# Optimization experiments

Measured on AMD Instinct MI355X. Metric: run time of the kernel, lower is better.

## Reference

```python
import jax, jax.numpy as jnp
import numpy as np

DIM, HEADS, WS, SS = 256, 8, 4, 2
B, D, H, W = 2, 16, 56, 56


def _rel_pos_index(ws):
    coords = np.stack(np.meshgrid(np.arange(ws), np.arange(ws), np.arange(ws), indexing='ij'))
    flat = coords.reshape(3, -1)                      # [3, n]
    rel = (flat[:, :, None] - flat[:, None, :]).transpose(1, 2, 0).astype(np.int64)  # [n,n,3]
    rel[..., 0] += ws - 1; rel[..., 1] += ws - 1; rel[..., 2] += ws - 1
    rel[..., 0] *= (2 * ws - 1) ** 2
    rel[..., 1] *= (2 * ws - 1)
    return rel.sum(-1)                                # [n, n]


def _attn_mask(d, h, w, ws, ss):
    # dims are divisible by ws here, so padded dims == dims (matches torch ceil-pad)
    img = np.zeros((d, h, w))
    sl = (slice(0, -ws), slice(-ws, -ss), slice(-ss, None))
    cnt = 0
    for dsl in sl:
        for hsl in sl:
            for wsl in sl:
                img[dsl, hsl, wsl] = cnt
                cnt += 1
    mw = img.reshape(d // ws, ws, h // ws, ws, w // ws, ws)
    mw = mw.transpose(0, 2, 4, 1, 3, 5).reshape(-1, ws ** 3)   # [nW, n]
    diff = mw[:, None, :] - mw[:, :, None]
    return np.where(diff != 0, -100.0, 0.0).astype(np.float32)  # [nW, n, n]


def _window_partition(x, ws):
    b, d, h, w, c = x.shape
    x = x.reshape(b, d // ws, ws, h // ws, ws, w // ws, ws, c)
    return x.transpose(0, 1, 3, 5, 2, 4, 6, 7).reshape(-1, ws ** 3, c)


def _window_reverse(win, ws, b, d, h, w, c):
    x = win.reshape(b, d // ws, h // ws, w // ws, ws, ws, ws, c)
    return x.transpose(0, 1, 4, 2, 5, 3, 6, 7).reshape(b, d, h, w, c)


def _ln(x, g, b, eps=1e-5):
    mu = x.mean(-1, keepdims=True)
    var = ((x - mu) ** 2).mean(-1, keepdims=True)
    return (x - mu) * jax.lax.rsqrt(var + eps) * g + b


def setup_inputs() -> dict:
    key = jax.random.key(0)
    ks = jax.random.split(key, 8)
    s = 0.02
    return {
        'x': jax.random.normal(ks[0], (B, D, H, W, DIM), jnp.float32),
        'norm1_g': jnp.ones((DIM,), jnp.float32),
        'norm1_b': jnp.zeros((DIM,), jnp.float32),
        'qkv_w': jax.random.normal(ks[1], (DIM, 3 * DIM), jnp.float32) * s,
        'qkv_b': jnp.zeros((3 * DIM,), jnp.float32),
        'proj_w': jax.random.normal(ks[2], (DIM, DIM), jnp.float32) * s,
        'proj_b': jnp.zeros((DIM,), jnp.float32),
        'rpb_table': jax.random.normal(ks[3], ((2 * WS - 1) ** 3, HEADS), jnp.float32) * s,
        'norm2_g': jnp.ones((DIM,), jnp.float32),
        'norm2_b': jnp.zeros((DIM,), jnp.float32),
        'fc1_w': jax.random.normal(ks[4], (DIM, 4 * DIM), jnp.float32) * s,
        'fc1_b': jnp.zeros((4 * DIM,), jnp.float32),
        'fc2_w': jax.random.normal(ks[5], (4 * DIM, DIM), jnp.float32) * s,
        'fc2_b': jnp.zeros((DIM,), jnp.float32),
    }


def reference(x, norm1_g, norm1_b, qkv_w, qkv_b, proj_w, proj_b, rpb_table,
              norm2_g, norm2_b, fc1_w, fc1_b, fc2_w, fc2_b):
    b, d, h, w, c = x.shape
    nh, ws, ss = HEADS, WS, SS
    hd = c // nh
    shortcut = x

    xn = _ln(x, norm1_g, norm1_b)
    xs = jnp.roll(xn, shift=(-ss, -ss, -ss), axis=(1, 2, 3))
    xw = _window_partition(xs, ws)            # [B_, n, c]
    B_, n, _ = xw.shape

    qkv = (xw @ qkv_w + qkv_b).reshape(B_, n, 3, nh, hd).transpose(2, 0, 3, 1, 4)
    q, k, v = qkv[0], qkv[1], qkv[2]          # [B_, nh, n, hd]
    attn = jnp.einsum('bhqd,bhkd->bhqk', q * (hd ** -0.5), k)

    rpi = jnp.asarray(_rel_pos_index(ws).reshape(-1))
    bias = rpb_table[rpi].reshape(n, n, nh).transpose(2, 0, 1)  # [nh, n, n]
    attn = attn + bias[None]

    mask = jnp.asarray(_attn_mask(d, h, w, ws, ss))             # [nW, n, n]
    nW = mask.shape[0]
    attn = attn.reshape(B_ // nW, nW, nh, n, n) + mask[None, :, None]
    attn = jax.nn.softmax(attn.reshape(B_, nh, n, n), axis=-1)

    out = jnp.einsum('bhqk,bhkd->bhqd', attn, v).transpose(0, 2, 1, 3).reshape(B_, n, c)
    out = out @ proj_w + proj_b

    xr = _window_reverse(out, ws, b, d, h, w, c)
    xr = jnp.roll(xr, shift=(ss, ss, ss), axis=(1, 2, 3))
    x1 = shortcut + xr

    y = _ln(x1, norm2_g, norm2_b)
    y = jax.nn.gelu(y @ fc1_w + fc1_b, approximate=False) @ fc2_w + fc2_b
    return x1 + y
```

## Files before the change

kernel.cpp:

```cpp
#include <hip/hip_runtime.h>
#include <math.h>


using f32x4  = __attribute__((ext_vector_type(4))) float;
using bf16x8 = __attribute__((ext_vector_type(8))) short;

#define MFMA16 __builtin_amdgcn_mfma_f32_16x16x32_bf16

__device__ __forceinline__ short f2bf(float f) {
  unsigned u = __builtin_bit_cast(unsigned, f);
  u += 0x7fffu + ((u >> 16) & 1u);
  return (short)(u >> 16);
}

__device__ __forceinline__ float gelu_f(float v) {
  const float u = 1.5957691216057308f * v * (1.f + 0.044715f * v * v);
  const float e = __expf(u);
  return v - v * __builtin_amdgcn_rcpf(e + 1.f);
}

#define GLDS16(g, l) __builtin_amdgcn_global_load_lds(                        \
    (__attribute__((address_space(1))) void*)(g),                             \
    (__attribute__((address_space(3))) void*)(l), 16, 0, 0)

__global__ void transpose_all_k(const float* __restrict__ qkv_w,
                                const float* __restrict__ proj_w,
                                const float* __restrict__ fc1_w,
                                const float* __restrict__ fc2_w,
                                short* __restrict__ o_qkv,
                                short* __restrict__ o_proj,
                                short* __restrict__ o_fc1,
                                short* __restrict__ o_fc2) {
  int bid = blockIdx.x;
  const float* in; short* out; int K, N;
  if (bid < 768)       { in = qkv_w;  out = o_qkv;  K = 256;  N = 768; }
  else if (bid < 1024) { in = proj_w; out = o_proj; K = 256;  N = 256;  bid -= 768; }
  else if (bid < 2048) { in = fc1_w;  out = o_fc1;  K = 256;  N = 1024; bid -= 1024; }
  else                 { in = fc2_w;  out = o_fc2;  K = 1024; N = 256;  bid -= 2048; }
  const int idx = bid * 256 + threadIdx.x;
  const int k = idx / N, n = idx % N;
  out[(size_t)n * K + k] = f2bf(in[idx]);
}

__global__ __launch_bounds__(256) void ln1_part_k(
    const float* __restrict__ x, const float* __restrict__ g,
    const float* __restrict__ bta, short* __restrict__ xw) {
  const int wave = threadIdx.x >> 6, lane = threadIdx.x & 63;
  const int row = blockIdx.x * 4 + wave;
  const int win = row >> 6, tok = row & 63;
  const int b = win / 784, wi = win % 784;
  const int wd = wi / 196, wh = (wi / 14) % 14, ww = wi % 14;
  const int tz = tok >> 4, ty = (tok >> 2) & 3, tx = tok & 3;
  const int gd = (wd * 4 + tz + 2) & 15;
  int gh = wh * 4 + ty + 2; if (gh >= 56) gh -= 56;
  int gw = ww * 4 + tx + 2; if (gw >= 56) gw -= 56;
  const size_t src = ((((size_t)b * 16 + gd) * 56 + gh) * 56 + gw) * 256;
  const float4 v = ((const float4*)(x + src))[lane];
  float s = v.x + v.y + v.z + v.w;
#pragma unroll
  for (int m = 1; m < 64; m <<= 1) s += __shfl_xor(s, m);
  const float mean = s * (1.f / 256.f);
  const float dx = v.x - mean, dy = v.y - mean, dz = v.z - mean, dw = v.w - mean;
  float q = dx * dx + dy * dy + dz * dz + dw * dw;
#pragma unroll
  for (int m = 1; m < 64; m <<= 1) q += __shfl_xor(q, m);
  const float rstd = rsqrtf(q * (1.f / 256.f) + 1e-5f);
  const float4 gg = ((const float4*)g)[lane];
  const float4 bb = ((const float4*)bta)[lane];
  short4 o;
  o.x = f2bf(dx * rstd * gg.x + bb.x);
  o.y = f2bf(dy * rstd * gg.y + bb.y);
  o.z = f2bf(dz * rstd * gg.z + bb.z);
  o.w = f2bf(dw * rstd * gg.w + bb.w);
  *(short4*)(xw + (size_t)row * 256 + lane * 4) = o;
}

__global__ __launch_bounds__(256) void ln2_k(
    const float* __restrict__ x1, const float* __restrict__ g,
    const float* __restrict__ bta, short* __restrict__ yn) {
  const int wave = threadIdx.x >> 6, lane = threadIdx.x & 63;
  const int row = blockIdx.x * 4 + wave;
  const float4 v = ((const float4*)(x1 + (size_t)row * 256))[lane];
  float s = v.x + v.y + v.z + v.w;
#pragma unroll
  for (int m = 1; m < 64; m <<= 1) s += __shfl_xor(s, m);
  const float mean = s * (1.f / 256.f);
  const float dx = v.x - mean, dy = v.y - mean, dz = v.z - mean, dw = v.w - mean;
  float q = dx * dx + dy * dy + dz * dz + dw * dw;
#pragma unroll
  for (int m = 1; m < 64; m <<= 1) q += __shfl_xor(q, m);
  const float rstd = rsqrtf(q * (1.f / 256.f) + 1e-5f);
  const float4 gg = ((const float4*)g)[lane];
  const float4 bb = ((const float4*)bta)[lane];
  short4 o;
  o.x = f2bf(dx * rstd * gg.x + bb.x);
  o.y = f2bf(dy * rstd * gg.y + bb.y);
  o.z = f2bf(dz * rstd * gg.z + bb.z);
  o.w = f2bf(dw * rstd * gg.w + bb.w);
  *(short4*)(yn + (size_t)row * 256 + lane * 4) = o;
}

template <int EPI>
__global__ __launch_bounds__(256) void gemm_k(
    const short* __restrict__ A, const short* __restrict__ Bt,
    const float* __restrict__ bias, const float* __restrict__ resid,
    void* __restrict__ OutP, int N, int K) {
  __shared__ short SMEM[32768];
  const int tid = threadIdx.x;
  const int wave = tid >> 6, lane = tid & 63;
  const int quad = lane >> 4, l15 = lane & 15;
  const int m0 = blockIdx.y * 128;
  const int n0 = blockIdx.x * 128;
  const int wm = (wave >> 1) * 64, wn = (wave & 1) * 64;

  f32x4 acc[4][4] = {};

  auto stage = [&](int b, int kk) {
    short* Asb = SMEM + b * 16384;
    short* Bsb = Asb + 8192;
#pragma unroll
    for (int i = 0; i < 4; ++i) {
      const int p = wave * 256 + i * 64 + lane;
      const int row = p >> 3;
      const int c = (p & 7) ^ (row & 7);
      GLDS16(A  + (size_t)(m0 + row) * K + (kk + c * 8),
             Asb + (size_t)(wave * 256 + i * 64) * 8);
      GLDS16(Bt + (size_t)(n0 + row) * K + (kk + c * 8),
             Bsb + (size_t)(wave * 256 + i * 64) * 8);
    }
  };
  auto compute = [&](int b) {
    const short* Asb = SMEM + b * 16384;
    const short* Bsb = Asb + 8192;
#pragma unroll
    for (int ks = 0; ks < 2; ++ks) {
      bf16x8 af[4], bfr[4];
#pragma unroll
      for (int t = 0; t < 4; ++t) {
        const int ra = wm + t * 16 + l15;
        const int ca = (ks * 4 + quad) ^ (ra & 7);
        af[t] = *(const bf16x8*)(Asb + ra * 64 + ca * 8);
        const int rb = wn + t * 16 + l15;
        const int cb = (ks * 4 + quad) ^ (rb & 7);
        bfr[t] = *(const bf16x8*)(Bsb + rb * 64 + cb * 8);
      }
#pragma unroll
      for (int mt = 0; mt < 4; ++mt)
#pragma unroll
        for (int nt = 0; nt < 4; ++nt)
          acc[mt][nt] = MFMA16(af[mt], bfr[nt], acc[mt][nt], 0, 0, 0);
    }
  };

  stage(0, 0);
  __syncthreads();
  int cur = 0;
  const int NT = K >> 6;
  for (int t = 0; t < NT - 1; ++t) {
    stage(cur ^ 1, (t + 1) * 64);
    compute(cur);
    __syncthreads();
    cur ^= 1;
  }
  compute(cur);

  __syncthreads();
  if constexpr (EPI == 0 || EPI == 1) {
#pragma unroll
    for (int nt = 0; nt < 4; ++nt) {
      const int col = wn + nt * 16 + l15;
      const float bv = bias[n0 + col];
#pragma unroll
      for (int mt = 0; mt < 4; ++mt)
#pragma unroll
        for (int reg = 0; reg < 4; ++reg) {
          const int row = wm + mt * 16 + quad * 4 + reg;
          float v = acc[mt][nt][reg] + bv;
          if constexpr (EPI == 1) v = gelu_f(v);
          const int byte = (row << 8) | ((col << 1) ^ ((row & 7) << 4));
          *(short*)((char*)SMEM + byte) = f2bf(v);
        }
    }
    __syncthreads();
    short* out = (short*)OutP;
#pragma unroll
    for (int i = 0; i < 8; ++i) {
      const int off = i * 4096 + tid * 16;
      const int row = off >> 8;
      const bf16x8 val =
          *(const bf16x8*)((char*)SMEM + (off ^ ((row & 7) << 4)));
      *(bf16x8*)(out + (size_t)(m0 + row) * N + n0 + ((off & 255) >> 1)) = val;
    }
  } else {
    float* out = (float*)OutP;
#pragma unroll
    for (int hh = 0; hh < 2; ++hh) {
      if (hh) __syncthreads();
      if (wm == hh * 64) {
#pragma unroll
        for (int nt = 0; nt < 4; ++nt) {
          const int col = wn + nt * 16 + l15;
          const float bv = bias[n0 + col];
#pragma unroll
          for (int mt = 0; mt < 4; ++mt)
#pragma unroll
            for (int reg = 0; reg < 4; ++reg) {
              const int rloc = mt * 16 + quad * 4 + reg;
              const int byte = (rloc << 9) | ((col << 2) ^ ((rloc & 7) << 4));
              *(float*)((char*)SMEM + byte) = acc[mt][nt][reg] + bv;
            }
        }
      }
      __syncthreads();
#pragma unroll
      for (int i = 0; i < 8; ++i) {
        const int off = i * 4096 + tid * 16;
        const int rloc = off >> 9;
        f32x4 val = *(const f32x4*)((char*)SMEM + (off ^ ((rloc & 7) << 4)));
        const int colf = (off & 511) >> 2;
        const int grow = m0 + hh * 64 + rloc;
        size_t dst;
        if constexpr (EPI == 2) {
          const int win = grow >> 6, tok = grow & 63;
          const int b = win / 784, wi = win % 784;
          const int wd = wi / 196, wh = (wi / 14) % 14, ww = wi % 14;
          const int tz = tok >> 4, ty = (tok >> 2) & 3, tx = tok & 3;
          const int gd = (wd * 4 + tz + 2) & 15;
          int gh = wh * 4 + ty + 2; if (gh >= 56) gh -= 56;
          int gw = ww * 4 + tx + 2; if (gw >= 56) gw -= 56;
          dst = ((((size_t)b * 16 + gd) * 56 + gh) * 56 + gw) * 256
                + n0 + colf;
        } else {
          dst = (size_t)grow * 256 + n0 + colf;
        }
        const f32x4 r = *(const f32x4*)(resid + dst);
        val = val + r;
        *(f32x4*)(out + dst) = val;
      }
    }
  }
}

__global__ __launch_bounds__(256) void attn_k(
    const short* __restrict__ qkv, const float* __restrict__ rpb,
    short* __restrict__ aout) {
  __shared__ short Plds[4 * 64 * 80];
  const int tid = threadIdx.x;
  const int wave = tid >> 6, lane = tid & 63;
  const int quad = lane >> 4, l15 = lane & 15;
  const int win = blockIdx.x >> 1;
  const int h = ((blockIdx.x & 1) << 2) + wave;
  const int wi = win % 784;
  const int wd = wi / 196, wh = (wi / 14) % 14, ww = wi % 14;
  const short* base = qkv + (size_t)win * (64 * 768);

  bf16x8 qf[4], kf[4];
#pragma unroll
  for (int t = 0; t < 4; ++t) {
    const short* qp = base + (size_t)(t * 16 + l15) * 768 + h * 32 + quad * 8;
    qf[t] = *(const bf16x8*)qp;
    kf[t] = *(const bf16x8*)(qp + 256);
  }
  f32x4 S[4][4] = {};
#pragma unroll
  for (int mt = 0; mt < 4; ++mt)
#pragma unroll
    for (int nt = 0; nt < 4; ++nt)
      S[mt][nt] = MFMA16(qf[mt], kf[nt], S[mt][nt], 0, 0, 0);

  const bool bd = (wd == 3), bh = (wh == 13), bw = (ww == 13);
  const int yc = l15 >> 2, xc = l15 & 3;
  int labc[4];
#pragma unroll
  for (int nt = 0; nt < 4; ++nt) {
    const int rd = bd ? (nt < 2 ? 1 : 2) : 0;
    const int rh = bh ? (yc < 2 ? 1 : 2) : 0;
    const int rw = bw ? (xc < 2 ? 1 : 2) : 0;
    labc[nt] = rd * 9 + rh * 3 + rw;
  }
  const float scale = 0.17677669529663687f;
#pragma unroll
  for (int mt = 0; mt < 4; ++mt) {
    const int rdr = bd ? (mt < 2 ? 1 : 2) : 0;
    const int rhr = bh ? (quad < 2 ? 1 : 2) : 0;
#pragma unroll
    for (int reg = 0; reg < 4; ++reg) {
      const int rwr = bw ? (reg < 2 ? 1 : 2) : 0;
      const int labr = rdr * 9 + rhr * 3 + rwr;
      float sc[4];
#pragma unroll
      for (int nt = 0; nt < 4; ++nt) {
        const int rpi = (mt - nt + 3) * 49 + (quad - yc + 3) * 7 + (reg - xc + 3);
        const float bias = rpb[rpi * 8 + h];
        const float mv = (labr == labc[nt]) ? 0.f : -100.f;
        sc[nt] = S[mt][nt][reg] * scale + bias + mv;
      }
      float mx = fmaxf(fmaxf(sc[0], sc[1]), fmaxf(sc[2], sc[3]));
      mx = fmaxf(mx, __shfl_xor(mx, 1));
      mx = fmaxf(mx, __shfl_xor(mx, 2));
      mx = fmaxf(mx, __shfl_xor(mx, 4));
      mx = fmaxf(mx, __shfl_xor(mx, 8));
      float p[4], sum = 0.f;
#pragma unroll
      for (int nt = 0; nt < 4; ++nt) { p[nt] = __expf(sc[nt] - mx); sum += p[nt]; }
      sum += __shfl_xor(sum, 1);
      sum += __shfl_xor(sum, 2);
      sum += __shfl_xor(sum, 4);
      sum += __shfl_xor(sum, 8);
      const float inv = 1.f / sum;
      const int r = mt * 16 + quad * 4 + reg;
#pragma unroll
      for (int nt = 0; nt < 4; ++nt)
        Plds[(wave * 64 + r) * 80 + nt * 16 + l15] = f2bf(p[nt] * inv);
    }
  }

  bf16x8 vf[2][2];
#pragma unroll
  for (int kt = 0; kt < 2; ++kt)
#pragma unroll
    for (int n2 = 0; n2 < 2; ++n2)
#pragma unroll
      for (int j = 0; j < 8; ++j)
        vf[kt][n2][j] =
            base[(size_t)(kt * 32 + quad * 8 + j) * 768 + 512 + h * 32 + n2 * 16 + l15];

  f32x4 O[4][2] = {};
#pragma unroll
  for (int mt = 0; mt < 4; ++mt) {
    const short* pr = &Plds[(wave * 64 + mt * 16 + l15) * 80 + quad * 8];
    const bf16x8 pa0 = *(const bf16x8*)pr;
    const bf16x8 pa1 = *(const bf16x8*)(pr + 32);
#pragma unroll
    for (int n2 = 0; n2 < 2; ++n2) {
      O[mt][n2] = MFMA16(pa0, vf[0][n2], O[mt][n2], 0, 0, 0);
      O[mt][n2] = MFMA16(pa1, vf[1][n2], O[mt][n2], 0, 0, 0);
    }
  }
#pragma unroll
  for (int mt = 0; mt < 4; ++mt)
#pragma unroll
    for (int n2 = 0; n2 < 2; ++n2)
#pragma unroll
      for (int reg = 0; reg < 4; ++reg) {
        const int tok = mt * 16 + quad * 4 + reg;
        aout[((size_t)win * 64 + tok) * 256 + h * 32 + n2 * 16 + l15] =
            f2bf(O[mt][n2][reg]);
      }
}

extern "C" void kernel_launch(void* const* d_in, const int* in_sizes, int n_in,
                              void* d_out, int out_size, void* d_ws,
                              size_t ws_size, hipStream_t stream) {
  const float* x      = (const float*)d_in[0];
  const float* n1g    = (const float*)d_in[1];
  const float* n1b    = (const float*)d_in[2];
  const float* qkv_w  = (const float*)d_in[3];
  const float* qkv_b  = (const float*)d_in[4];
  const float* proj_w = (const float*)d_in[5];
  const float* proj_b = (const float*)d_in[6];
  const float* rpb    = (const float*)d_in[7];
  const float* n2g    = (const float*)d_in[8];
  const float* n2b    = (const float*)d_in[9];
  const float* fc1_w  = (const float*)d_in[10];
  const float* fc1_b  = (const float*)d_in[11];
  const float* fc2_w  = (const float*)d_in[12];
  const float* fc2_b  = (const float*)d_in[13];

  char* ws = (char*)d_ws;
  short* wt_qkv  = (short*)(ws + 0);
  short* wt_proj = (short*)(ws + 393216);
  short* wt_fc1  = (short*)(ws + 524288);
  short* wt_fc2  = (short*)(ws + 1048576);
  short* bufS    = (short*)(ws + 1572864);
  short* bufL    = (short*)(ws + 52953088);
  float* x1      = (float*)d_out;

  transpose_all_k<<<3072, 256, 0, stream>>>(qkv_w, proj_w, fc1_w, fc2_w,
                                            wt_qkv, wt_proj, wt_fc1, wt_fc2);
  ln1_part_k<<<25088, 256, 0, stream>>>(x, n1g, n1b, bufS);
  gemm_k<0><<<dim3(6, 784), 256, 0, stream>>>(bufS, wt_qkv, qkv_b, nullptr,
                                              bufL, 768, 256);
  attn_k<<<3136, 256, 0, stream>>>(bufL, rpb, bufS);
  gemm_k<2><<<dim3(2, 784), 256, 0, stream>>>(bufS, wt_proj, proj_b, x,
                                              x1, 256, 256);
  ln2_k<<<25088, 256, 0, stream>>>(x1, n2g, n2b, bufS);
  gemm_k<1><<<dim3(8, 784), 256, 0, stream>>>(bufS, wt_fc1, fc1_b, nullptr,
                                              bufL, 1024, 256);
  gemm_k<3><<<dim3(2, 784), 256, 0, stream>>>(bufL, wt_fc2, fc2_b, x1,
                                              x1, 256, 1024);
}
```

Before: 666.8 us.

## Fuse LayerNorm1 into QKV GEMM and proj GEMM with LayerNorm2 per window

Replaces the separate ln1 partition kernel plus QKV GEMM with one kernel per window that normalizes 64 tokens into LDS and multiplies directly with the QKV weights. It also fuses the projection GEMM, residual add, window-reverse scatter and LayerNorm2 into one per-window kernel that writes both x1 and the normalized bf16 activations. This removes two intermediate bf16 activation round trips through HBM and two launches. In exchange, the fused GEMMs read B fragments straight from global memory without LDS staging or double buffering, and the 64-row tiles lower data reuse.

```diff
diff --git a/kernel.cpp b/kernel.cpp
--- a/kernel.cpp
+++ b/kernel.cpp
@@ -22,6 +22,16 @@
 #define GLDS16(g, l) __builtin_amdgcn_global_load_lds(                        \
     (__attribute__((address_space(1))) void*)(g),                             \
     (__attribute__((address_space(3))) void*)(l), 16, 0, 0)
+
+__device__ __forceinline__ size_t swin_src(int win, int tok) {
+  const int b = win / 784, wi = win % 784;
+  const int wd = wi / 196, wh = (wi / 14) % 14, ww = wi % 14;
+  const int tz = tok >> 4, ty = (tok >> 2) & 3, tx = tok & 3;
+  const int gd = (wd * 4 + tz + 2) & 15;
+  int gh = wh * 4 + ty + 2; if (gh >= 56) gh -= 56;
+  int gw = ww * 4 + tx + 2; if (gw >= 56) gw -= 56;
+  return ((((size_t)b * 16 + gd) * 56 + gh) * 56 + gw) * 256;
+}
 
 __global__ void transpose_all_k(const float* __restrict__ qkv_w,
                                 const float* __restrict__ proj_w,
@@ -42,62 +52,214 @@
   out[(size_t)n * K + k] = f2bf(in[idx]);
 }
 
-__global__ __launch_bounds__(256) void ln1_part_k(
+__global__ __launch_bounds__(512) void ln1qkv_k(
     const float* __restrict__ x, const float* __restrict__ g,
-    const float* __restrict__ bta, short* __restrict__ xw) {
-  const int wave = threadIdx.x >> 6, lane = threadIdx.x & 63;
-  const int row = blockIdx.x * 4 + wave;
-  const int win = row >> 6, tok = row & 63;
-  const int b = win / 784, wi = win % 784;
-  const int wd = wi / 196, wh = (wi / 14) % 14, ww = wi % 14;
-  const int tz = tok >> 4, ty = (tok >> 2) & 3, tx = tok & 3;
-  const int gd = (wd * 4 + tz + 2) & 15;
-  int gh = wh * 4 + ty + 2; if (gh >= 56) gh -= 56;
-  int gw = ww * 4 + tx + 2; if (gw >= 56) gw -= 56;
-  const size_t src = ((((size_t)b * 16 + gd) * 56 + gh) * 56 + gw) * 256;
-  const float4 v = ((const float4*)(x + src))[lane];
-  float s = v.x + v.y + v.z + v.w;
-#pragma unroll
-  for (int m = 1; m < 64; m <<= 1) s += __shfl_xor(s, m);
+    const float* __restrict__ bta, const short* __restrict__ Wq,
+    const float* __restrict__ qb, short* __restrict__ qkv) {
+  __shared__ __align__(16) char SM[32768];
+  const int tid = threadIdx.x;
+  const int win = blockIdx.x;
+
+  {
+    const int tk = tid >> 3, lane3 = tid & 7;
+    const size_t src = swin_src(win, tk);
+    f32x4 xr[8];
+#pragma unroll
+    for (int i = 0; i < 8; ++i)
+      xr[i] = *(const f32x4*)(x + src + lane3 * 32 + i * 4);
+    float s = 0.f;
+#pragma unroll
+    for (int i = 0; i < 8; ++i) s += xr[i][0] + xr[i][1] + xr[i][2] + xr[i][3];
+    s += __shfl_xor(s, 1); s += __shfl_xor(s, 2); s += __shfl_xor(s, 4);
+    const float mean = s * (1.f / 256.f);
+    float q = 0.f;
+#pragma unroll
+    for (int i = 0; i < 8; ++i)
+#pragma unroll
+      for (int j = 0; j < 4; ++j) {
+        const float d = xr[i][j] - mean; q += d * d;
+      }
+    q += __shfl_xor(q, 1); q += __shfl_xor(q, 2); q += __shfl_xor(q, 4);
+    const float rstd = rsqrtf(q * (1.f / 256.f) + 1e-5f);
+#pragma unroll
+    for (int cc = 0; cc < 4; ++cc) {
+      const float4 g0 = *(const float4*)(g + lane3 * 32 + cc * 8);
+      const float4 g1 = *(const float4*)(g + lane3 * 32 + cc * 8 + 4);
+      const float4 b0 = *(const float4*)(bta + lane3 * 32 + cc * 8);
+      const float4 b1 = *(const float4*)(bta + lane3 * 32 + cc * 8 + 4);
+      const f32x4 va = xr[cc * 2], vb = xr[cc * 2 + 1];
+      bf16x8 o;
+      o[0] = f2bf((va[0] - mean) * rstd * g0.x + b0.x);
+      o[1] = f2bf((va[1] - mean) * rstd * g0.y + b0.y);
+      o[2] = f2bf((va[2] - mean) * rstd * g0.z + b0.z);
+      o[3] = f2bf((va[3] - mean) * rstd * g0.w + b0.w);
+      o[4] = f2bf((vb[0] - mean) * rstd * g1.x + b1.x);
+      o[5] = f2bf((vb[1] - mean) * rstd * g1.y + b1.y);
+      o[6] = f2bf((vb[2] - mean) * rstd * g1.z + b1.z);
+      o[7] = f2bf((vb[3] - mean) * rstd * g1.w + b1.w);
+      const int byte = tk * 512 + (((lane3 * 4 + cc) ^ (tk & 7)) << 4);
+      *(bf16x8*)(SM + byte) = o;
+    }
+  }
+  __syncthreads();
+
+  const int wave = tid >> 6, lane = tid & 63;
+  const int quad = lane >> 4, l15 = lane & 15;
+  const int h = wave;
+  f32x4 acc[3][2][4] = {};
+#pragma unroll
+  for (int kk = 0; kk < 8; ++kk) {
+    bf16x8 af[4];
+#pragma unroll
+    for (int mt = 0; mt < 4; ++mt) {
+      const int t = mt * 16 + l15;
+      const int byte = t * 512 + (((kk * 4 + quad) ^ (t & 7)) << 4);
+      af[mt] = *(const bf16x8*)(SM + byte);
+    }
+#pragma unroll
+    for (int gq = 0; gq < 3; ++gq)
+#pragma unroll
+      for (int ct = 0; ct < 2; ++ct) {
+        const int col = gq * 256 + h * 32 + ct * 16 + l15;
+        const bf16x8 bfr =
+            *(const bf16x8*)(Wq + (size_t)col * 256 + kk * 32 + quad * 8);
+#pragma unroll
+        for (int mt = 0; mt < 4; ++mt)
+          acc[gq][ct][mt] = MFMA16(af[mt], bfr, acc[gq][ct][mt], 0, 0, 0);
+      }
+  }
+
+  short* const outp = qkv + (size_t)win * 64 * 768;
+#pragma unroll
+  for (int gq = 0; gq < 3; ++gq) {
+    __syncthreads();
+#pragma unroll
+    for (int ct = 0; ct < 2; ++ct)
+#pragma unroll
+      for (int mt = 0; mt < 4; ++mt)
+#pragma unroll
+        for (int reg = 0; reg < 4; ++reg) {
+          const int t = mt * 16 + quad * 4 + reg;
+          const int col = h * 32 + ct * 16 + l15;
+          const float v = acc[gq][ct][mt][reg] + qb[gq * 256 + col];
+          const int cb = col * 2;
+          const int byte = t * 512 + (((cb >> 4) ^ (t & 7)) << 4) + (cb & 15);
+          *(short*)(SM + byte) = f2bf(v);
+        }
+    __syncthreads();
+#pragma unroll
+    for (int i = 0; i < 4; ++i) {
+      const int off = i * 8192 + tid * 16;
+      const int row = off >> 9, cb = off & 511;
+      const bf16x8 val = *(const bf16x8*)(SM + (off ^ ((row & 7) << 4)));
+      *(bf16x8*)(outp + (size_t)row * 768 + gq * 256 + (cb >> 1)) = val;
+    }
+  }
+}
+
+__global__ __launch_bounds__(256) void projln2_k(
+    const short* __restrict__ ao, const short* __restrict__ Wp,
+    const float* __restrict__ pb, const float* __restrict__ xres,
+    const float* __restrict__ g2, const float* __restrict__ b2,
+    float* __restrict__ x1, short* __restrict__ yn) {
+  __shared__ __align__(16) char SM[65536];
+  const int tid = threadIdx.x;
+  const int wave = tid >> 6, lane = tid & 63;
+  const int quad = lane >> 4, l15 = lane & 15;
+  const int m0 = blockIdx.x * 64;
+
+#pragma unroll
+  for (int i = 0; i < 8; ++i) {
+    const int p = i * 256 + tid;
+    const int row = p >> 5;
+    const int c = (p & 31) ^ (row & 7);
+    GLDS16(ao + (size_t)(m0 + row) * 256 + c * 8, SM + p * 16);
+  }
+  __syncthreads();
+
+  f32x4 pacc[4][4] = {};
+#pragma unroll
+  for (int kk = 0; kk < 8; ++kk) {
+    bf16x8 af[4];
+#pragma unroll
+    for (int mt = 0; mt < 4; ++mt) {
+      const int t = mt * 16 + l15;
+      const int byte = t * 512 + (((kk * 4 + quad) ^ (t & 7)) << 4);
+      af[mt] = *(const bf16x8*)(SM + byte);
+    }
+#pragma unroll
+    for (int nt = 0; nt < 4; ++nt) {
+      const int col = wave * 64 + nt * 16 + l15;
+      const bf16x8 bfr =
+          *(const bf16x8*)(Wp + (size_t)col * 256 + kk * 32 + quad * 8);
+#pragma unroll
+      for (int mt = 0; mt < 4; ++mt)
+        pacc[mt][nt] = MFMA16(af[mt], bfr, pacc[mt][nt], 0, 0, 0);
+    }
+  }
+
+  __syncthreads();
+#pragma unroll
+  for (int nt = 0; nt < 4; ++nt) {
+    const int col = wave * 64 + nt * 16 + l15;
+    const float bv = pb[col];
+#pragma unroll
+    for (int mt = 0; mt < 4; ++mt)
+#pragma unroll
+      for (int reg = 0; reg < 4; ++reg) {
+        const int t = mt * 16 + quad * 4 + reg;
+        const int byte =
+            t * 1024 + ((((col >> 2)) ^ (t & 7)) << 4) + (col & 3) * 4;
+        *(float*)(SM + byte) = pacc[mt][nt][reg] + bv;
+      }
+  }
+  __syncthreads();
+
+  const int tok = tid >> 2, lane2 = tid & 3;
+  const size_t src = swin_src(blockIdx.x, tok);
+  f32x4 x1v[16];
+  float s = 0.f;
+#pragma unroll
+  for (int cc = 0; cc < 16; ++cc) {
+    const int ch = lane2 * 16 + cc;
+    f32x4 v = *(const f32x4*)(SM + tok * 1024 + ((ch ^ (tok & 7)) << 4));
+    const f32x4 r = *(const f32x4*)(xres + src + lane2 * 64 + cc * 4);
+    v = v + r;
+    x1v[cc] = v;
+    s += v[0] + v[1] + v[2] + v[3];
+  }
+  s += __shfl_xor(s, 1); s += __shfl_xor(s, 2);
   const float mean = s * (1.f / 256.f);
-  const float dx = v.x - mean, dy = v.y - mean, dz = v.z - mean, dw = v.w - mean;
-  float q = dx * dx + dy * dy + dz * dz + dw * dw;
-#pragma unroll
-  for (int m = 1; m < 64; m <<= 1) q += __shfl_xor(q, m);
+  float q = 0.f;
+#pragma unroll
+  for (int cc = 0; cc < 16; ++cc)
+#pragma unroll
+    for (int j = 0; j < 4; ++j) {
+      const float d = x1v[cc][j] - mean; q += d * d;
+    }
+  q += __shfl_xor(q, 1); q += __shfl_xor(q, 2);
   const float rstd = rsqrtf(q * (1.f / 256.f) + 1e-5f);
-  const float4 gg = ((const float4*)g)[lane];
-  const float4 bb = ((const float4*)bta)[lane];
-  short4 o;
-  o.x = f2bf(dx * rstd * gg.x + bb.x);
-  o.y = f2bf(dy * rstd * gg.y + bb.y);
-  o.z = f2bf(dz * rstd * gg.z + bb.z);
-  o.w = f2bf(dw * rstd * gg.w + bb.w);
-  *(short4*)(xw + (size_t)row * 256 + lane * 4) = o;
-}
-
-__global__ __launch_bounds__(256) void ln2_k(
-    const float* __restrict__ x1, const float* __restrict__ g,
-    const float* __restrict__ bta, short* __restrict__ yn) {
-  const int wave = threadIdx.x >> 6, lane = threadIdx.x & 63;
-  const int row = blockIdx.x * 4 + wave;
-  const float4 v = ((const float4*)(x1 + (size_t)row * 256))[lane];
-  float s = v.x + v.y + v.z + v.w;
-#pragma unroll
-  for (int m = 1; m < 64; m <<= 1) s += __shfl_xor(s, m);
-  const float mean = s * (1.f / 256.f);
-  const float dx = v.x - mean, dy = v.y - mean, dz = v.z - mean, dw = v.w - mean;
-  float q = dx * dx + dy * dy + dz * dz + dw * dw;
-#pragma unroll
-  for (int m = 1; m < 64; m <<= 1) q += __shfl_xor(q, m);
-  const float rstd = rsqrtf(q * (1.f / 256.f) + 1e-5f);
-  const float4 gg = ((const float4*)g)[lane];
-  const float4 bb = ((const float4*)bta)[lane];
-  short4 o;
-  o.x = f2bf(dx * rstd * gg.x + bb.x);
-  o.y = f2bf(dy * rstd * gg.y + bb.y);
-  o.z = f2bf(dz * rstd * gg.z + bb.z);
-  o.w = f2bf(dw * rstd * gg.w + bb.w);
-  *(short4*)(yn + (size_t)row * 256 + lane * 4) = o;
+#pragma unroll
+  for (int cc = 0; cc < 16; ++cc)
+    *(f32x4*)(x1 + src + lane2 * 64 + cc * 4) = x1v[cc];
+#pragma unroll
+  for (int u = 0; u < 8; ++u) {
+    const float4 gA = *(const float4*)(g2 + lane2 * 64 + u * 8);
+    const float4 gB = *(const float4*)(g2 + lane2 * 64 + u * 8 + 4);
+    const float4 bA = *(const float4*)(b2 + lane2 * 64 + u * 8);
+    const float4 bB = *(const float4*)(b2 + lane2 * 64 + u * 8 + 4);
+    const f32x4 va = x1v[u * 2], vb = x1v[u * 2 + 1];
+    bf16x8 o;
+    o[0] = f2bf((va[0] - mean) * rstd * gA.x + bA.x);
+    o[1] = f2bf((va[1] - mean) * rstd * gA.y + bA.y);
+    o[2] = f2bf((va[2] - mean) * rstd * gA.z + bA.z);
+    o[3] = f2bf((va[3] - mean) * rstd * gA.w + bA.w);
+    o[4] = f2bf((vb[0] - mean) * rstd * gB.x + bB.x);
+    o[5] = f2bf((vb[1] - mean) * rstd * gB.y + bB.y);
+    o[6] = f2bf((vb[2] - mean) * rstd * gB.z + bB.z);
+    o[7] = f2bf((vb[3] - mean) * rstd * gB.w + bB.w);
+    *(bf16x8*)(yn + src + lane2 * 64 + u * 8) = o;
+  }
 }
 
 template <int EPI>
@@ -165,7 +327,7 @@
   compute(cur);
 
   __syncthreads();
-  if constexpr (EPI == 0 || EPI == 1) {
+  if constexpr (EPI == 1) {
 #pragma unroll
     for (int nt = 0; nt < 4; ++nt) {
       const int col = wn + nt * 16 + l15;
@@ -175,8 +337,7 @@
 #pragma unroll
         for (int reg = 0; reg < 4; ++reg) {
           const int row = wm + mt * 16 + quad * 4 + reg;
-          float v = acc[mt][nt][reg] + bv;
-          if constexpr (EPI == 1) v = gelu_f(v);
+          float v = gelu_f(acc[mt][nt][reg] + bv);
           const int byte = (row << 8) | ((col << 1) ^ ((row & 7) << 4));
           *(short*)((char*)SMEM + byte) = f2bf(v);
         }
@@ -218,21 +379,7 @@
         const int rloc = off >> 9;
         f32x4 val = *(const f32x4*)((char*)SMEM + (off ^ ((rloc & 7) << 4)));
         const int colf = (off & 511) >> 2;
-        const int grow = m0 + hh * 64 + rloc;
-        size_t dst;
-        if constexpr (EPI == 2) {
-          const int win = grow >> 6, tok = grow & 63;
-          const int b = win / 784, wi = win % 784;
-          const int wd = wi / 196, wh = (wi / 14) % 14, ww = wi % 14;
-          const int tz = tok >> 4, ty = (tok >> 2) & 3, tx = tok & 3;
-          const int gd = (wd * 4 + tz + 2) & 15;
-          int gh = wh * 4 + ty + 2; if (gh >= 56) gh -= 56;
-          int gw = ww * 4 + tx + 2; if (gw >= 56) gw -= 56;
-          dst = ((((size_t)b * 16 + gd) * 56 + gh) * 56 + gw) * 256
-                + n0 + colf;
-        } else {
-          dst = (size_t)grow * 256 + n0 + colf;
-        }
+        const size_t dst = (size_t)(m0 + hh * 64 + rloc) * 256 + n0 + colf;
         const f32x4 r = *(const f32x4*)(resid + dst);
         val = val + r;
         *(f32x4*)(out + dst) = val;
@@ -374,18 +521,16 @@
   short* wt_fc2  = (short*)(ws + 1048576);
   short* bufS    = (short*)(ws + 1572864);
   short* bufL    = (short*)(ws + 52953088);
+  short* bufY    = (short*)(ws + 258473984);
   float* x1      = (float*)d_out;
 
   transpose_all_k<<<3072, 256, 0, stream>>>(qkv_w, proj_w, fc1_w, fc2_w,
                                             wt_qkv, wt_proj, wt_fc1, wt_fc2);
-  ln1_part_k<<<25088, 256, 0, stream>>>(x, n1g, n1b, bufS);
-  gemm_k<0><<<dim3(6, 784), 256, 0, stream>>>(bufS, wt_qkv, qkv_b, nullptr,
-                                              bufL, 768, 256);
+  ln1qkv_k<<<1568, 512, 0, stream>>>(x, n1g, n1b, wt_qkv, qkv_b, bufL);
   attn_k<<<3136, 256, 0, stream>>>(bufL, rpb, bufS);
-  gemm_k<2><<<dim3(2, 784), 256, 0, stream>>>(bufS, wt_proj, proj_b, x,
-                                              x1, 256, 256);
-  ln2_k<<<25088, 256, 0, stream>>>(x1, n2g, n2b, bufS);
-  gemm_k<1><<<dim3(8, 784), 256, 0, stream>>>(bufS, wt_fc1, fc1_b, nullptr,
+  projln2_k<<<1568, 256, 0, stream>>>(bufS, wt_proj, proj_b, x, n2g, n2b,
+                                      x1, bufY);
+  gemm_k<1><<<dim3(8, 784), 256, 0, stream>>>(bufY, wt_fc1, fc1_b, nullptr,
                                               bufL, 1024, 256);
   gemm_k<3><<<dim3(2, 784), 256, 0, stream>>>(bufL, wt_fc2, fc2_b, x1,
                                               x1, 256, 1024);
```

After: 770.7 us. 15.6% more time.

## Store QKV head-major per window and XCD-swizzle the fc1 GEMM grid

Applied to the files above, without the earlier changes.

The QKV GEMM epilogue now writes its output as [window][head][q/k/v][64 tokens][32 dims], so each attention wave reads contiguous 4 KB blocks for its head instead of strided rows of width 768. This is meant to make the Q/K/V loads in the attention kernel, especially the scalar V gathers, coalesced. Separately, the fc1 GEMM remaps block indices in groups of 8 (the XSWZ template flag). The intent is to place neighbouring tiles on the same XCD and improve L2 reuse of the A and B tiles. The remap assumes the total block count is divisible by 8, which holds for the 8x784 fc1 grid.

```diff
diff --git a/kernel.cpp b/kernel.cpp
--- a/kernel.cpp
+++ b/kernel.cpp
@@ -100,7 +100,7 @@
   *(short4*)(yn + (size_t)row * 256 + lane * 4) = o;
 }
 
-template <int EPI>
+template <int EPI, int XSWZ>
 __global__ __launch_bounds__(256) void gemm_k(
     const short* __restrict__ A, const short* __restrict__ Bt,
     const float* __restrict__ bias, const float* __restrict__ resid,
@@ -109,8 +109,18 @@
   const int tid = threadIdx.x;
   const int wave = tid >> 6, lane = tid & 63;
   const int quad = lane >> 4, l15 = lane & 15;
-  const int m0 = blockIdx.y * 128;
-  const int n0 = blockIdx.x * 128;
+  int m0, n0;
+  if constexpr (XSWZ) {
+    const int gx = gridDim.x;
+    int lin = blockIdx.y * gx + blockIdx.x;
+    const int q8 = (gx * gridDim.y) >> 3;
+    lin = (lin & 7) * q8 + (lin >> 3);
+    m0 = (lin / gx) * 128;
+    n0 = (lin % gx) * 128;
+  } else {
+    m0 = blockIdx.y * 128;
+    n0 = blockIdx.x * 128;
+  }
   const int wm = (wave >> 1) * 64, wn = (wave & 1) * 64;
 
   f32x4 acc[4][4] = {};
@@ -189,7 +199,17 @@
       const int row = off >> 8;
       const bf16x8 val =
           *(const bf16x8*)((char*)SMEM + (off ^ ((row & 7) << 4)));
-      *(bf16x8*)(out + (size_t)(m0 + row) * N + n0 + ((off & 255) >> 1)) = val;
+      if constexpr (EPI == 0) {
+        const int colg = n0 + ((off & 255) >> 1);
+        const int gq = colg >> 8, rem = colg & 255;
+        const int hh = rem >> 5, dd = rem & 31;
+        const int grow = m0 + row;
+        const int win = grow >> 6, tok = grow & 63;
+        *(bf16x8*)(out + ((((size_t)win * 8 + hh) * 3 + gq) << 11)
+                       + tok * 32 + dd) = val;
+      } else {
+        *(bf16x8*)(out + (size_t)(m0 + row) * N + n0 + ((off & 255) >> 1)) = val;
+      }
     }
   } else {
     float* out = (float*)OutP;
@@ -252,14 +272,13 @@
   const int h = ((blockIdx.x & 1) << 2) + wave;
   const int wi = win % 784;
   const int wd = wi / 196, wh = (wi / 14) % 14, ww = wi % 14;
-  const short* base = qkv + (size_t)win * (64 * 768);
+  const short* base = qkv + ((((size_t)win * 8 + h) * 3) << 11);
 
   bf16x8 qf[4], kf[4];
 #pragma unroll
   for (int t = 0; t < 4; ++t) {
-    const short* qp = base + (size_t)(t * 16 + l15) * 768 + h * 32 + quad * 8;
-    qf[t] = *(const bf16x8*)qp;
-    kf[t] = *(const bf16x8*)(qp + 256);
+    qf[t] = *(const bf16x8*)(base + (t * 16 + l15) * 32 + quad * 8);
+    kf[t] = *(const bf16x8*)(base + 2048 + (t * 16 + l15) * 32 + quad * 8);
   }
   f32x4 S[4][4] = {};
 #pragma unroll
@@ -323,7 +342,7 @@
 #pragma unroll
       for (int j = 0; j < 8; ++j)
         vf[kt][n2][j] =
-            base[(size_t)(kt * 32 + quad * 8 + j) * 768 + 512 + h * 32 + n2 * 16 + l15];
+            base[4096 + (kt * 32 + quad * 8 + j) * 32 + n2 * 16 + l15];
 
   f32x4 O[4][2] = {};
 #pragma unroll
@@ -379,14 +398,14 @@
   transpose_all_k<<<3072, 256, 0, stream>>>(qkv_w, proj_w, fc1_w, fc2_w,
                                             wt_qkv, wt_proj, wt_fc1, wt_fc2);
   ln1_part_k<<<25088, 256, 0, stream>>>(x, n1g, n1b, bufS);
-  gemm_k<0><<<dim3(6, 784), 256, 0, stream>>>(bufS, wt_qkv, qkv_b, nullptr,
-                                              bufL, 768, 256);
+  gemm_k<0, 0><<<dim3(6, 784), 256, 0, stream>>>(bufS, wt_qkv, qkv_b, nullptr,
+                                                 bufL, 768, 256);
   attn_k<<<3136, 256, 0, stream>>>(bufL, rpb, bufS);
-  gemm_k<2><<<dim3(2, 784), 256, 0, stream>>>(bufS, wt_proj, proj_b, x,
-                                              x1, 256, 256);
+  gemm_k<2, 0><<<dim3(2, 784), 256, 0, stream>>>(bufS, wt_proj, proj_b, x,
+                                                 x1, 256, 256);
   ln2_k<<<25088, 256, 0, stream>>>(x1, n2g, n2b, bufS);
-  gemm_k<1><<<dim3(8, 784), 256, 0, stream>>>(bufS, wt_fc1, fc1_b, nullptr,
-                                              bufL, 1024, 256);
-  gemm_k<3><<<dim3(2, 784), 256, 0, stream>>>(bufL, wt_fc2, fc2_b, x1,
-                                              x1, 256, 1024);
-}
+  gemm_k<1, 1><<<dim3(8, 784), 256, 0, stream>>>(bufS, wt_fc1, fc1_b, nullptr,
+                                                 bufL, 1024, 256);
+  gemm_k<3, 0><<<dim3(2, 784), 256, 0, stream>>>(bufL, wt_fc2, fc2_b, x1,
+                                                 x1, 256, 1024);
+}
```

New measurement: 659.7 us. About the same (-1.1%).
